# Kernel tuning notes

Hardware: AMD Instinct MI355X
Metric: run time of the kernel (lower is better)

## Reference

```python
import jax, jax.numpy as jnp
import numpy as np

LAMBDA_A = 1.0
NUM_ITER = 3
K = 64
BN_EPS = 1e-5


def setup_inputs() -> dict:
    key = jax.random.key(0)
    ks = jax.random.split(key, 8)
    B, C, H, W = 16, 512, 64, 64
    x = jax.random.normal(ks[0], (B, C, H, W), dtype=jnp.float32)
    # codebook mu: init normal(std~sqrt(2/k)) then L2-normalize along dim=1 (k axis), as in torch init
    mu = jax.random.normal(ks[1], (C, K), dtype=jnp.float32) * np.sqrt(2.0 / K)
    mu = mu / jnp.maximum(jnp.linalg.norm(mu, axis=1, keepdims=True), 1e-12)
    # 1x1 convs expressed as (out, in) matrices
    stem_w = jax.random.normal(ks[2], (C, C), dtype=jnp.float32) * np.sqrt(2.0 / C)
    stem_b = jnp.zeros((C,), dtype=jnp.float32)
    head_w = jax.random.normal(ks[3], (C, C), dtype=jnp.float32) * np.sqrt(2.0 / C)
    head_b = jnp.zeros((C,), dtype=jnp.float32)
    bn_gamma = jnp.ones((C,), dtype=jnp.float32)
    bn_beta = jnp.zeros((C,), dtype=jnp.float32)
    return {"x": x, "mu": mu, "stem_w": stem_w, "stem_b": stem_b,
            "head_w": head_w, "head_b": head_b,
            "bn_gamma": bn_gamma, "bn_beta": bn_beta}


def _conv1x1(x, w, b):
    # x: (B,C,H,W), w: (O,C)
    return jnp.einsum('bchw,oc->bohw', x, w) + b[None, :, None, None]


def reference(x, mu, stem_w, stem_b, head_w, head_b, bn_gamma, bn_beta):
    B, C, H, W = x.shape
    N = H * W
    y = _conv1x1(x, stem_w, stem_b)                 # (B,C,H,W)
    yf = y.reshape(B, C, N).transpose(0, 2, 1)      # (B,N,C)

    mu_b = jnp.broadcast_to(mu[None], (B, C, K))    # (B,C,K)
    z = None
    for _ in range(NUM_ITER):
        z = jax.nn.softmax(LAMBDA_A * jnp.einsum('bnc,bck->bnk', yf, mu_b), axis=2)
        zn = z / (1e-6 + z.sum(axis=1, keepdims=True))
        mu_b = jnp.einsum('bnc,bnk->bck', yf, zn)
        mu_b = mu_b / jnp.maximum(jnp.linalg.norm(mu_b, axis=1, keepdims=True), 1e-12)

    # EM loop runs under no_grad in torch
    mu_b = jax.lax.stop_gradient(mu_b)
    z = jax.lax.stop_gradient(z)

    y2 = jnp.einsum('bck,bnk->bcn', mu_b, z).reshape(B, C, H, W)

    # head: ReLU -> 1x1 conv -> BatchNorm2d (training-mode batch stats)
    h = _conv1x1(jnp.maximum(y2, 0.0), head_w, head_b)
    mean = h.mean(axis=(0, 2, 3), keepdims=True)
    var = h.var(axis=(0, 2, 3), keepdims=True)
    h = (h - mean) * jax.lax.rsqrt(var + BN_EPS)
    h = h * bn_gamma[None, :, None, None] + bn_beta[None, :, None, None]

    return jnp.maximum(h + x, 0.0)
```

## Files before the change

kernel.cpp:

```cpp
#include <hip/hip_runtime.h>


typedef _Float16 half_t;
typedef _Float16 half4 __attribute__((ext_vector_type(4)));
typedef _Float16 half8 __attribute__((ext_vector_type(8)));
typedef float f32x4 __attribute__((ext_vector_type(4)));

#define GLD_LDS(gp, lp) __builtin_amdgcn_global_load_lds( \
    (const __attribute__((address_space(1))) void*)(gp),  \
    (__attribute__((address_space(3))) void*)(lp), 16, 0, 0)

#define SBAR __builtin_amdgcn_sched_barrier(0)
#define RAWBAR do { SBAR; __builtin_amdgcn_s_barrier(); SBAR; } while (0)
#define LGKM0 do { asm volatile("s_waitcnt lgkmcnt(0)" ::: "memory"); SBAR; } while (0)

template <int L> __device__ __forceinline__ void vmwait() {
  if constexpr (L == 8) asm volatile("s_waitcnt vmcnt(8)" ::: "memory");
  else if constexpr (L == 6) asm volatile("s_waitcnt vmcnt(6)" ::: "memory");
  else if constexpr (L == 4) asm volatile("s_waitcnt vmcnt(4)" ::: "memory");
  else asm volatile("s_waitcnt vmcnt(0)" ::: "memory");
}

constexpr int CB = 16;
constexpr int CC = 512;
constexpr int CN = 4096;
constexpr int CKK = 64;
constexpr long MALL = (long)CB * CN;

__device__ inline int swz8(int bid, int n) {
  return (bid & 7) * (n >> 3) + (bid >> 3);
}

__global__ __launch_bounds__(256) void prep(
    const float* __restrict__ stem_w, const float* __restrict__ head_w,
    const float* __restrict__ mu,
    half_t* __restrict__ swh, half_t* __restrict__ hwh,
    half_t* __restrict__ muT, half_t* __restrict__ muck)
{
  int i = blockIdx.x * 256 + threadIdx.x;
  swh[i] = (half_t)stem_w[i];
  hwh[i] = (half_t)head_w[i];
  if (i < CC * CKK) {
    int c = i >> 6, k = i & 63;
    half_t v = (half_t)mu[i];
    for (int b = 0; b < CB; ++b) {
      muT[(long)b * CKK * CC + (long)k * CC + c] = v;
      muck[(long)b * CC * CKK + i] = v;
    }
  }
}

template <bool SWZ>
__global__ __launch_bounds__(256) void gemm_stem(
    const float* __restrict__ X, const half_t* __restrict__ Bw,
    const float* __restrict__ bias,
    half_t* __restrict__ Co, half_t* __restrict__ CoT)
{
  constexpr int SAB = 16384;
  __shared__ __align__(16) half_t smem[2 * SAB];
  const int tid = threadIdx.x, wid = tid >> 6, lane = tid & 63;
  int bid = blockIdx.x;
  if constexpr (SWZ) bid = swz8(bid, gridDim.x);
  const int tm = bid >> 2, tn = bid & 3;
  const long row0 = (long)tm * 128;
  const long b = row0 >> 12;
  const int n0 = (int)(row0 & 4095);
  const float* Xb = X + b * ((long)CC * CN) + n0;
  const half_t* Bb = Bw + (long)tn * 128 * CC;
  const int wr = wid >> 1, wc = wid & 1;

  const int an = tid & 127;
  const int ac0 = (tid >> 7) * 32;
  const int r8 = lane >> 3;
  const int gcs = ((lane & 7) ^ r8) * 8;

  float va[32];
  auto issueA = [&](int ks) {
    const float* p = Xb + (long)(ks * 64 + ac0) * CN + an;
#pragma unroll
    for (int e = 0; e < 32; ++e) va[e] = p[(long)e * CN];
  };
  auto writeA = [&](int buf) {
    half_t* dA = smem + buf * SAB;
#pragma unroll
    for (int g = 0; g < 4; ++g) {
      half8 h;
#pragma unroll
      for (int e = 0; e < 8; ++e) h[e] = (half_t)va[g * 8 + e];
      const int chunk = (ac0 >> 3) + g;
      *(half8*)&dA[an * 64 + ((chunk ^ (an & 7)) << 3)] = h;
    }
  };
  auto stageB = [&](int ks, int buf) {
    half_t* dB = smem + buf * SAB + 8192;
    const half_t* gb = Bb + (long)ks * 64;
#pragma unroll
    for (int c = wid; c < 16; c += 4)
      GLD_LDS(gb + (long)(c * 8 + r8) * CC + gcs, &dB[c * 512]);
  };

  f32x4 acc[4][4];
#pragma unroll
  for (int i = 0; i < 4; ++i)
#pragma unroll
    for (int j = 0; j < 4; ++j) acc[i][j] = f32x4{0.f, 0.f, 0.f, 0.f};

  issueA(0);
  stageB(0, 0);
  vmwait<0>();
  writeA(0);
  LGKM0;
  RAWBAR;

  int cur = 0;
  for (int ks = 0; ks < 8; ++ks) {
    if (ks < 7) { issueA(ks + 1); stageB(ks + 1, cur ^ 1); }
    const half_t* lA = smem + cur * SAB;
    const half_t* lB = lA + 8192;
#pragma unroll
    for (int kk = 0; kk < 2; ++kk) {
      half8 af[4], bfr[4];
      const int cg = kk * 4 + (lane >> 4);
#pragma unroll
      for (int i = 0; i < 4; ++i) {
        const int rA = wr * 64 + i * 16 + (lane & 15);
        af[i] = *(const half8*)&lA[rA * 64 + ((cg ^ (rA & 7)) << 3)];
      }
#pragma unroll
      for (int j = 0; j < 4; ++j) {
        const int rB = wc * 64 + j * 16 + (lane & 15);
        bfr[j] = *(const half8*)&lB[rB * 64 + ((cg ^ (rB & 7)) << 3)];
      }
      __builtin_amdgcn_s_setprio(1);
#pragma unroll
      for (int i = 0; i < 4; ++i)
#pragma unroll
        for (int j = 0; j < 4; ++j)
          acc[i][j] = __builtin_amdgcn_mfma_f32_16x16x32_f16(af[i], bfr[j],
                                                             acc[i][j], 0, 0, 0);
      __builtin_amdgcn_s_setprio(0);
    }
    RAWBAR;
    if (ks < 7) {
      vmwait<0>();
      writeA(cur ^ 1);
      LGKM0;
    }
    RAWBAR;
    cur ^= 1;
  }

  constexpr int PIT = 132;
  half_t* ep = smem;
#pragma unroll
  for (int j = 0; j < 4; ++j) {
    const int nl = wc * 64 + j * 16 + (lane & 15);
    const float bv = bias[tn * 128 + nl];
#pragma unroll
    for (int i = 0; i < 4; ++i) {
      const int ml = wr * 64 + i * 16 + ((lane >> 4) << 2);
      half4 h;
#pragma unroll
      for (int r = 0; r < 4; ++r) h[r] = (half_t)(acc[i][j][r] + bv);
      *(half4*)&ep[nl * PIT + ml] = h;
    }
  }
  __syncthreads();
  {
#pragma unroll
    for (int s = 0; s < 8; ++s) {
      const int q = tid + 256 * s;
      const int m = q & 127, cc8 = q >> 7;
      half8 v;
#pragma unroll
      for (int e = 0; e < 8; ++e) v[e] = ep[(cc8 * 8 + e) * PIT + m];
      *(half8*)&Co[(row0 + m) * CC + tn * 128 + cc8 * 8] = v;
    }
  }
  {
#pragma unroll
    for (int s = 0; s < 8; ++s) {
      const int q = tid + 256 * s;
      const int mc = q & 15, cl = q >> 4;
      half8 v = *(const half8*)&ep[cl * PIT + mc * 8];
      *(half8*)&CoT[(b * CC + tn * 128 + cl) * CN + n0 + mc * 8] = v;
    }
  }
}

template <int BM, int BN, int MODE, int EPI, bool SWZ, bool STATS>
__global__ __launch_bounds__(256) void gemm_abt(
    const half_t* __restrict__ A, const half_t* __restrict__ Bm,
    half_t* __restrict__ Co, half_t* __restrict__ CoT,
    float* __restrict__ Cacc, const float* __restrict__ bias,
    float* __restrict__ stats,
    int M, int Nn, int Kk, int ksplit, long sA, long sB, long sC)
{
  constexpr int FM = BM / 32, FN = BN / 32;
  constexpr int HB = (BM + BN) * 64;
  constexpr int LCNT = (BM / 8) / 4 + (BN / 8) / 4;
  constexpr int STG = 2 * HB;
  constexpr int EPS = (EPI != 0) ? BN * (BM + 4) : 0;
  constexpr int TOT = STG > EPS ? STG : EPS;
  __shared__ __align__(16) half_t smem[TOT];

  const int tid = threadIdx.x, wid = tid >> 6, lane = tid & 63;
  int bid = blockIdx.x;
  if constexpr (SWZ) bid = swz8(bid, gridDim.x);
  const int tilesN = Nn / BN;
  const int tm = bid / tilesN, tn = bid % tilesN;
  const long bz = blockIdx.z;
  const half_t* Ab = A + bz * sA + (long)tm * BM * Kk;
  const half_t* Bb = Bm + bz * sB + (long)tn * BN * Kk;
  const int ksteps = Kk >> 6;
  const int per = ksteps / ksplit;
  const int ks0 = blockIdx.y * per, ks1 = ks0 + per;
  const int wr = wid >> 1, wc = wid & 1;

  const int r8 = lane >> 3;
  const int gcs = ((lane & 7) ^ r8) * 8;

  auto stage = [&](int ks, int buf) {
    half_t* dA = smem + buf * HB;
    half_t* dB = dA + BM * 64;
    const half_t* ga = Ab + (long)ks * 64;
#pragma unroll
    for (int c = wid; c < BM / 8; c += 4)
      GLD_LDS(ga + (long)(c * 8 + r8) * Kk + gcs, &dA[c * 512]);
    const half_t* gb = Bb + (long)ks * 64;
#pragma unroll
    for (int c = wid; c < BN / 8; c += 4)
      GLD_LDS(gb + (long)(c * 8 + r8) * Kk + gcs, &dB[c * 512]);
  };

  f32x4 acc[FM][FN];
#pragma unroll
  for (int i = 0; i < FM; ++i)
#pragma unroll
    for (int j = 0; j < FN; ++j) acc[i][j] = f32x4{0.f, 0.f, 0.f, 0.f};

  stage(ks0, 0);
  if (ks0 + 1 < ks1) { stage(ks0 + 1, 1); vmwait<LCNT>(); }
  else               { vmwait<0>(); }
  RAWBAR;

  int cur = 0;
  for (int ks = ks0; ks < ks1; ++ks) {
    const half_t* lA = smem + cur * HB;
    const half_t* lB = lA + BM * 64;
#pragma unroll
    for (int kk = 0; kk < 2; ++kk) {
      half8 af[FM], bfr[FN];
      const int cg = kk * 4 + (lane >> 4);
#pragma unroll
      for (int i = 0; i < FM; ++i) {
        const int rA = wr * (BM / 2) + i * 16 + (lane & 15);
        af[i] = *(const half8*)&lA[rA * 64 + ((cg ^ (rA & 7)) << 3)];
      }
#pragma unroll
      for (int j = 0; j < FN; ++j) {
        const int rB = wc * (BN / 2) + j * 16 + (lane & 15);
        bfr[j] = *(const half8*)&lB[rB * 64 + ((cg ^ (rB & 7)) << 3)];
      }
      __builtin_amdgcn_s_setprio(1);
#pragma unroll
      for (int i = 0; i < FM; ++i)
#pragma unroll
        for (int j = 0; j < FN; ++j)
          acc[i][j] = __builtin_amdgcn_mfma_f32_16x16x32_f16(af[i], bfr[j],
                                                             acc[i][j], 0, 0, 0);
      __builtin_amdgcn_s_setprio(0);
    }
    RAWBAR;
    const bool more = (ks + 2 < ks1);
    if (more) { stage(ks + 2, cur); vmwait<LCNT>(); }
    else      { vmwait<0>(); }
    RAWBAR;
    cur ^= 1;
  }

  if constexpr (EPI != 0) {
    static_assert(BM == 128 && BN == 128, "LDS epilogue assumes 128x128");
    constexpr int PIT = BM + 4;
    half_t* ep = smem;
#pragma unroll
    for (int j = 0; j < FN; ++j) {
      const int nl = wc * 64 + j * 16 + (lane & 15);
      float bv = 0.f;
      if constexpr (MODE & 1) bv = bias[tn * BN + nl];
      float s1 = 0.f, s2 = 0.f;
#pragma unroll
      for (int i = 0; i < FM; ++i) {
        const int ml = wr * 64 + i * 16 + ((lane >> 4) << 2);
        half4 h;
#pragma unroll
        for (int r = 0; r < 4; ++r) {
          float v = acc[i][j][r] + bv;
          if constexpr (MODE & 2) v = fmaxf(v, 0.f);
          if constexpr (STATS) { s1 += v; s2 += v * v; }
          h[r] = (half_t)v;
        }
        *(half4*)&ep[nl * PIT + ml] = h;
      }
      if constexpr (STATS) {
        s1 += __shfl_xor(s1, 16); s1 += __shfl_xor(s1, 32);
        s2 += __shfl_xor(s2, 16); s2 += __shfl_xor(s2, 32);
        if (lane < 16) {
          const int ch = tn * BN + nl;
          atomicAdd(&stats[ch], s1);
          atomicAdd(&stats[CC + ch], s2);
        }
      }
    }
    __syncthreads();
    const long rowbase = (long)tm * BM;
    if constexpr (EPI & 1) {
#pragma unroll
      for (int s = 0; s < 8; ++s) {
        const int q = tid + 256 * s;
        const int m = q & 127, cc8 = q >> 7;
        half8 v;
#pragma unroll
        for (int e = 0; e < 8; ++e) v[e] = ep[(cc8 * 8 + e) * PIT + m];
        *(half8*)&Co[bz * sC + (rowbase + m) * Nn + tn * BN + cc8 * 8] = v;
      }
    }
    if constexpr (EPI & 2) {
      const long b = rowbase >> 12, nbase = rowbase & 4095;
#pragma unroll
      for (int s = 0; s < 8; ++s) {
        const int q = tid + 256 * s;
        const int mc = q & 15, cl = q >> 4;
        half8 v = *(const half8*)&ep[cl * PIT + mc * 8];
        *(half8*)&CoT[(b * Nn + tn * BN + cl) * 4096 + nbase + mc * 8] = v;
      }
    }
  } else {
#pragma unroll
    for (int j = 0; j < FN; ++j) {
      const int n = tn * BN + wc * (BN / 2) + j * 16 + (lane & 15);
      float bv = 0.f;
      if constexpr (MODE & 1) bv = bias[n];
#pragma unroll
      for (int i = 0; i < FM; ++i) {
        const int mbase = tm * BM + wr * (BM / 2) + i * 16 + ((lane >> 4) << 2);
#pragma unroll
        for (int r = 0; r < 4; ++r) {
          if constexpr ((MODE & 4) != 0) {
            const long idx = bz * sC + (long)blockIdx.y * ((long)BM * Nn) +
                             (long)(mbase + r) * Nn + n;
            Cacc[idx] = acc[i][j][r];
          } else {
            const long idx = bz * sC + (long)(mbase + r) * Nn + n;
            float v = acc[i][j][r] + bv;
            if constexpr ((MODE & 2) != 0) v = fmaxf(v, 0.f);
            Co[idx] = (half_t)v;
          }
        }
      }
    }
  }
}

__global__ __launch_bounds__(256) void s_softmax(
    const half_t* __restrict__ Yf, const half_t* __restrict__ muT,
    half_t* __restrict__ zp, half_t* __restrict__ zT)
{
  constexpr int HB = (128 + 64) * 64;
  __shared__ __align__(16) union {
    half_t st[2 * HB];
    half_t zh[128 * 68];
  } sm;
  const int tid = threadIdx.x, wid = tid >> 6, lane = tid & 63;
  const int tm = blockIdx.x;
  const long bz = blockIdx.z;
  const half_t* Ab = Yf + bz * (long)CN * CC + (long)tm * 128 * CC;
  const half_t* Bb = muT + bz * (long)CKK * CC;

  const int r8 = lane >> 3;
  const int gcs = ((lane & 7) ^ r8) * 8;

  auto stage = [&](int ks, int buf) {
    half_t* dA = sm.st + buf * HB;
    half_t* dB = dA + 128 * 64;
    const half_t* ga = Ab + (long)ks * 64;
#pragma unroll
    for (int c = wid; c < 16; c += 4)
      GLD_LDS(ga + (long)(c * 8 + r8) * CC + gcs, &dA[c * 512]);
    const half_t* gb = Bb + (long)ks * 64;
#pragma unroll
    for (int c = wid; c < 8; c += 4)
      GLD_LDS(gb + (long)(c * 8 + r8) * CC + gcs, &dB[c * 512]);
  };

  f32x4 acc[2][4];
#pragma unroll
  for (int i = 0; i < 2; ++i)
#pragma unroll
    for (int j = 0; j < 4; ++j) acc[i][j] = f32x4{0.f, 0.f, 0.f, 0.f};

  stage(0, 0);
  stage(1, 1);
  vmwait<6>();
  RAWBAR;
  int cur = 0;
  for (int ks = 0; ks < 8; ++ks) {
    const half_t* lA = sm.st + cur * HB;
    const half_t* lB = lA + 128 * 64;
#pragma unroll
    for (int kk = 0; kk < 2; ++kk) {
      half8 af[2], bfr[4];
      const int cg = kk * 4 + (lane >> 4);
#pragma unroll
      for (int i = 0; i < 2; ++i) {
        const int rA = wid * 32 + i * 16 + (lane & 15);
        af[i] = *(const half8*)&lA[rA * 64 + ((cg ^ (rA & 7)) << 3)];
      }
#pragma unroll
      for (int j = 0; j < 4; ++j) {
        const int rB = j * 16 + (lane & 15);
        bfr[j] = *(const half8*)&lB[rB * 64 + ((cg ^ (rB & 7)) << 3)];
      }
      __builtin_amdgcn_s_setprio(1);
#pragma unroll
      for (int i = 0; i < 2; ++i)
#pragma unroll
        for (int j = 0; j < 4; ++j)
          acc[i][j] = __builtin_amdgcn_mfma_f32_16x16x32_f16(af[i], bfr[j],
                                                             acc[i][j], 0, 0, 0);
      __builtin_amdgcn_s_setprio(0);
    }
    RAWBAR;
    const bool more = (ks + 2 < 8);
    if (more) { stage(ks + 2, cur); vmwait<6>(); }
    else      { vmwait<0>(); }
    RAWBAR;
    cur ^= 1;
  }

#pragma unroll
  for (int i = 0; i < 2; ++i)
#pragma unroll
    for (int r = 0; r < 4; ++r) {
      float mx = fmaxf(fmaxf(acc[i][0][r], acc[i][1][r]),
                       fmaxf(acc[i][2][r], acc[i][3][r]));
#pragma unroll
      for (int m = 1; m < 16; m <<= 1) mx = fmaxf(mx, __shfl_xor(mx, m));
      float p[4], s = 0.f;
#pragma unroll
      for (int j = 0; j < 4; ++j) { p[j] = __expf(acc[i][j][r] - mx); s += p[j]; }
#pragma unroll
      for (int m = 1; m < 16; m <<= 1) s += __shfl_xor(s, m);
      const float inv = 1.f / s;
#pragma unroll
      for (int j = 0; j < 4; ++j) acc[i][j][r] = p[j] * inv;
    }

#pragma unroll
  for (int i = 0; i < 2; ++i)
#pragma unroll
    for (int j = 0; j < 4; ++j)
#pragma unroll
      for (int r = 0; r < 4; ++r) {
        const int row = wid * 32 + i * 16 + ((lane >> 4) << 2) + r;
        const int col = j * 16 + (lane & 15);
        sm.zh[row * 68 + col] = (half_t)acc[i][j][r];
      }
  __syncthreads();
  if (zp) {
    const int nl = tid >> 1, seg = tid & 1;
    const long base = bz * (long)CN * CKK + (long)(tm * 128 + nl) * CKK + seg * 32;
#pragma unroll
    for (int g = 0; g < 4; ++g) {
      half8 v;
#pragma unroll
      for (int e = 0; e < 8; ++e) v[e] = sm.zh[nl * 68 + seg * 32 + g * 8 + e];
      *(half8*)&zp[base + g * 8] = v;
    }
  }
  {
    const int k = tid >> 2, seg = tid & 3;
    const long base = bz * (long)CKK * CN + (long)k * CN + tm * 128 + seg * 32;
#pragma unroll
    for (int g = 0; g < 4; ++g) {
      half8 v;
#pragma unroll
      for (int e = 0; e < 8; ++e) v[e] = sm.zh[(seg * 32 + g * 8 + e) * 68 + k];
      *(half8*)&zT[base + g * 8] = v;
    }
  }
}

__global__ __launch_bounds__(64) void mu_norm(
    const float* __restrict__ acc, half_t* __restrict__ muT, half_t* __restrict__ muck)
{
  const int bk = blockIdx.x;
  const int b = bk >> 6, k = bk & 63;
  const float* base = acc + ((long)b * 4 * CKK + k) * CC;
  const int t = threadIdx.x;
  float v[8]; float s = 0.f;
#pragma unroll
  for (int e = 0; e < 8; ++e) {
    float a = base[t * 8 + e] + base[CKK * CC + t * 8 + e] +
              base[2 * CKK * CC + t * 8 + e] + base[3 * CKK * CC + t * 8 + e];
    v[e] = a; s += a * a;
  }
#pragma unroll
  for (int m = 1; m < 64; m <<= 1) s += __shfl_xor(s, m);
  const float inv = 1.f / fmaxf(sqrtf(s), 1e-12f);
  half8 o;
#pragma unroll
  for (int e = 0; e < 8; ++e) o[e] = (half_t)(v[e] * inv);
  *(half8*)&muT[(long)bk * CC + t * 8] = o;
  half_t* mc = muck + (long)b * CC * CKK;
#pragma unroll
  for (int e = 0; e < 8; ++e) mc[(long)(t * 8 + e) * CKK + k] = o[e];
}

__global__ void bn_param(const float* __restrict__ stats,
                         const float* __restrict__ gamma, const float* __restrict__ beta,
                         float* __restrict__ scsh)
{
  const int c = threadIdx.x;
  const float cnt = 1.f / 65536.f;
  const float mean = stats[c] * cnt;
  const float var = stats[CC + c] * cnt - mean * mean;
  const float sc = gamma[c] * rsqrtf(var + 1e-5f);
  scsh[c] = sc;
  scsh[CC + c] = beta[c] - mean * sc;
}

__global__ __launch_bounds__(256) void bn_final2(
    const half_t* __restrict__ hcn, const float* __restrict__ x,
    const float* __restrict__ scsh, float* __restrict__ out)
{
  const long i8 = (long)blockIdx.x * 256 + threadIdx.x;
  const int c = (int)((i8 >> 9) & 511);
  const float sc = scsh[c], sh = scsh[CC + c];
  half8 h = *(const half8*)&hcn[i8 * 8];
  f32x4 x0 = *(const f32x4*)&x[i8 * 8];
  f32x4 x1 = *(const f32x4*)&x[i8 * 8 + 4];
  f32x4 o0, o1;
#pragma unroll
  for (int e = 0; e < 4; ++e) o0[e] = fmaxf((float)h[e] * sc + sh + x0[e], 0.f);
#pragma unroll
  for (int e = 0; e < 4; ++e) o1[e] = fmaxf((float)h[4 + e] * sc + sh + x1[e], 0.f);
  *(f32x4*)&out[i8 * 8] = o0;
  *(f32x4*)&out[i8 * 8 + 4] = o1;
}

extern "C" void kernel_launch(void* const* d_in, const int* in_sizes, int n_in,
                              void* d_out, int out_size, void* d_ws, size_t ws_size,
                              hipStream_t stream)
{
  const float* x      = (const float*)d_in[0];
  const float* mu     = (const float*)d_in[1];
  const float* stem_w = (const float*)d_in[2];
  const float* stem_b = (const float*)d_in[3];
  const float* head_w = (const float*)d_in[4];
  const float* head_b = (const float*)d_in[5];
  const float* bn_g   = (const float*)d_in[6];
  const float* bn_b   = (const float*)d_in[7];
  float* out = (float*)d_out;

  const size_t NEED = 214ull << 20;
  if (ws_size < NEED) {
    hipMemsetAsync(d_out, 0, (size_t)out_size * 4, stream);
    return;
  }
  char* ws = (char*)d_ws;
  const long MB = 1 << 20;
  half_t* y2f  = (half_t*)(ws);
  float* muacc = (float*)(ws);
  half_t* Yf   = (half_t*)(ws + 64 * MB);
  half_t* ycn  = (half_t*)(ws + 128 * MB);
  half_t* z    = (half_t*)(ws + 192 * MB);
  half_t* zT   = (half_t*)(ws + 200 * MB);
  half_t* muT  = (half_t*)(ws + 208 * MB);
  half_t* muck = (half_t*)(ws + 209 * MB);
  half_t* swh  = (half_t*)(ws + 212 * MB);
  half_t* hwh  = (half_t*)(ws + 212 * MB + 512 * 1024);
  float* stats = (float*)(ws + 213 * MB);
  float* scsh  = (float*)(ws + 213 * MB + 8 * 1024);
  half_t* hcn = Yf;

  prep<<<1024, 256, 0, stream>>>(stem_w, head_w, mu, swh, hwh, muT, muck);
  gemm_stem<true><<<2048, 256, 0, stream>>>(x, swh, stem_b, Yf, ycn);

  for (int it = 0; it < 3; ++it) {
    s_softmax<<<dim3(32, 1, 16), 256, 0, stream>>>(
        Yf, muT, (it == 2) ? z : nullptr, zT);
    gemm_abt<64, 128, 4, 0, false, false><<<dim3(4, 4, 16), 256, 0, stream>>>(
        zT, ycn, nullptr, nullptr, muacc, nullptr, nullptr, CKK, CC, CN, 4,
        (long)CKK * CN, (long)CC * CN, (long)4 * CKK * CC);
    mu_norm<<<CB * CKK, 64, 0, stream>>>(muacc, muT, muck);
  }
  gemm_abt<128, 128, 2, 1, true, false><<<dim3(128, 1, 16), 256, 0, stream>>>(
      z, muck, y2f, nullptr, nullptr, nullptr, nullptr, CN, CC, CKK, 1,
      (long)CN * CKK, (long)CC * CKK, (long)CN * CC);
  hipMemsetAsync(stats, 0, 2 * CC * sizeof(float), stream);
  gemm_abt<128, 128, 1, 2, true, true><<<dim3(2048, 1, 1), 256, 0, stream>>>(
      y2f, hwh, nullptr, hcn, nullptr, head_b, stats, (int)MALL, CC, CC, 1, 0, 0, 0);

  bn_param<<<1, 512, 0, stream>>>(stats, bn_g, bn_b, scsh);
  bn_final2<<<16384, 256, 0, stream>>>(hcn, x, scsh, out);
}
```

Baseline: 383.4 us.

## Split stem GEMM into fp16 transpose pass plus single-buffered async-LDS GEMM

```diff
diff --git a/kernel.cpp b/kernel.cpp
--- a/kernel.cpp
+++ b/kernel.cpp
@@ -50,49 +50,65 @@
   }
 }
 
-template <bool SWZ>
-__global__ __launch_bounds__(256) void gemm_stem(
-    const float* __restrict__ X, const half_t* __restrict__ Bw,
+__global__ __launch_bounds__(256) void xpose(
+    const float* __restrict__ in, half_t* __restrict__ outT)
+{
+  __shared__ half_t t[64][72];
+  const int n0 = blockIdx.x * 64, c0 = blockIdx.y * 64;
+  const long bz = blockIdx.z;
+  const float* ib = in + bz * (long)CC * CN;
+  half_t* ob = outT + bz * (long)CC * CN;
+  const int tid = threadIdx.x;
+  {
+    const int c = tid >> 2, l4 = tid & 3;
+    const float* p = ib + (long)(c0 + c) * CN + n0;
+#pragma unroll
+    for (int e = 0; e < 4; ++e) {
+      const int nq = (l4 + e * 4) * 4;
+      f32x4 v = *(const f32x4*)&p[nq];
+#pragma unroll
+      for (int j = 0; j < 4; ++j) t[c][nq + j] = (half_t)v[j];
+    }
+  }
+  __syncthreads();
+#pragma unroll
+  for (int e = 0; e < 2; ++e) {
+    const int q = e * 256 + tid;
+    const int n = q >> 3, c8 = (q & 7) * 8;
+    half8 v;
+#pragma unroll
+    for (int j = 0; j < 8; ++j) v[j] = t[c8 + j][n];
+    *(half8*)&ob[(long)(n0 + n) * CC + c0 + c8] = v;
+  }
+}
+
+__global__ __launch_bounds__(256) void gemm_sb(
+    const half_t* __restrict__ A, const half_t* __restrict__ Bw,
     const float* __restrict__ bias,
     half_t* __restrict__ Co, half_t* __restrict__ CoT)
 {
-  constexpr int SAB = 16384;
-  __shared__ __align__(16) half_t smem[2 * SAB];
+  constexpr int HB = 256 * 64;
+  constexpr int EPS = 128 * 132;
+  constexpr int TOT = HB > EPS ? HB : EPS;
+  __shared__ __align__(16) half_t smem[TOT];
+
   const int tid = threadIdx.x, wid = tid >> 6, lane = tid & 63;
-  int bid = blockIdx.x;
-  if constexpr (SWZ) bid = swz8(bid, gridDim.x);
+  const int bid = swz8(blockIdx.x, gridDim.x);
   const int tm = bid >> 2, tn = bid & 3;
-  const long row0 = (long)tm * 128;
-  const long b = row0 >> 12;
-  const int n0 = (int)(row0 & 4095);
-  const float* Xb = X + b * ((long)CC * CN) + n0;
+  const half_t* Ab = A + (long)tm * 128 * CC;
   const half_t* Bb = Bw + (long)tn * 128 * CC;
   const int wr = wid >> 1, wc = wid & 1;
 
-  const int an = tid & 127;
-  const int ac0 = (tid >> 7) * 32;
   const int r8 = lane >> 3;
   const int gcs = ((lane & 7) ^ r8) * 8;
 
-  float va[32];
-  auto issueA = [&](int ks) {
-    const float* p = Xb + (long)(ks * 64 + ac0) * CN + an;
-#pragma unroll
-    for (int e = 0; e < 32; ++e) va[e] = p[(long)e * CN];
-  };
-  auto writeA = [&](int buf) {
-    half_t* dA = smem + buf * SAB;
-#pragma unroll
-    for (int g = 0; g < 4; ++g) {
-      half8 h;
-#pragma unroll
-      for (int e = 0; e < 8; ++e) h[e] = (half_t)va[g * 8 + e];
-      const int chunk = (ac0 >> 3) + g;
-      *(half8*)&dA[an * 64 + ((chunk ^ (an & 7)) << 3)] = h;
-    }
-  };
-  auto stageB = [&](int ks, int buf) {
-    half_t* dB = smem + buf * SAB + 8192;
+  auto stage = [&](int ks) {
+    half_t* dA = smem;
+    half_t* dB = smem + 128 * 64;
+    const half_t* ga = Ab + (long)ks * 64;
+#pragma unroll
+    for (int c = wid; c < 16; c += 4)
+      GLD_LDS(ga + (long)(c * 8 + r8) * CC + gcs, &dA[c * 512]);
     const half_t* gb = Bb + (long)ks * 64;
 #pragma unroll
     for (int c = wid; c < 16; c += 4)
@@ -105,18 +121,12 @@
 #pragma unroll
     for (int j = 0; j < 4; ++j) acc[i][j] = f32x4{0.f, 0.f, 0.f, 0.f};
 
-  issueA(0);
-  stageB(0, 0);
-  vmwait<0>();
-  writeA(0);
-  LGKM0;
-  RAWBAR;
-
-  int cur = 0;
   for (int ks = 0; ks < 8; ++ks) {
-    if (ks < 7) { issueA(ks + 1); stageB(ks + 1, cur ^ 1); }
-    const half_t* lA = smem + cur * SAB;
-    const half_t* lB = lA + 8192;
+    stage(ks);
+    asm volatile("s_waitcnt vmcnt(0)" ::: "memory"); SBAR;
+    RAWBAR;
+    const half_t* lA = smem;
+    const half_t* lB = smem + 128 * 64;
 #pragma unroll
     for (int kk = 0; kk < 2; ++kk) {
       half8 af[4], bfr[4];
@@ -141,13 +151,6 @@
       __builtin_amdgcn_s_setprio(0);
     }
     RAWBAR;
-    if (ks < 7) {
-      vmwait<0>();
-      writeA(cur ^ 1);
-      LGKM0;
-    }
-    RAWBAR;
-    cur ^= 1;
   }
 
   constexpr int PIT = 132;
@@ -166,6 +169,9 @@
     }
   }
   __syncthreads();
+  const long row0 = (long)tm * 128;
+  const long b = row0 >> 12;
+  const int n0 = (int)(row0 & 4095);
   {
 #pragma unroll
     for (int s = 0; s < 8; ++s) {
@@ -570,8 +576,9 @@
   }
   char* ws = (char*)d_ws;
   const long MB = 1 << 20;
+  half_t* xT   = (half_t*)(ws);
+  float* muacc = (float*)(ws);
   half_t* y2f  = (half_t*)(ws);
-  float* muacc = (float*)(ws);
   half_t* Yf   = (half_t*)(ws + 64 * MB);
   half_t* ycn  = (half_t*)(ws + 128 * MB);
   half_t* z    = (half_t*)(ws + 192 * MB);
@@ -585,7 +592,8 @@
   half_t* hcn = Yf;
 
   prep<<<1024, 256, 0, stream>>>(stem_w, head_w, mu, swh, hwh, muT, muck);
-  gemm_stem<true><<<2048, 256, 0, stream>>>(x, swh, stem_b, Yf, ycn);
+  xpose<<<dim3(64, 8, 16), 256, 0, stream>>>(x, xT);
+  gemm_sb<<<2048, 256, 0, stream>>>(xT, swh, stem_b, Yf, ycn);
 
   for (int it = 0; it < 3; ++it) {
     s_softmax<<<dim3(32, 1, 16), 256, 0, stream>>>(
```

Result: slower. 398.9 us (+4.0%).
